# Optimization experiments

Measured on AMD Instinct MI355X. Metric: run time of the kernel, lower is better.

Reference implementation:

```python
import jax, jax.numpy as jnp
import numpy as np

VTHR = 1.0


def setup_inputs() -> dict:
    key = jax.random.key(0)
    k1, k2, k3 = jax.random.split(key, 3)
    B, T, IN, OUT = 256, 8, 4096, 4096
    x = jax.random.normal(k1, (B * T, IN), dtype=jnp.float32)
    weight_scaled = jax.random.normal(k2, (OUT, IN), dtype=jnp.float32) * 0.02
    bias_scaled = jax.random.normal(k3, (OUT,), dtype=jnp.float32) * 0.02
    return {"x": x, "weight_scaled": weight_scaled, "bias_scaled": bias_scaled, "timesteps": T}


def _spike_linear(x, weight_scaled, bias_scaled, timesteps):
    # F.linear: [B*T, IN] @ [OUT, IN]^T + [OUT]
    out = jnp.dot(x, weight_scaled.T) + bias_scaled  # [B*T, OUT]
    OUT = out.shape[-1]
    out_s = out.reshape(-1, timesteps, OUT)  # [B, T, OUT]
    out_t = jnp.transpose(out_s, (1, 0, 2))  # [T, B, OUT] for scan

    def step(memb, o_t):
        memb = memb + VTHR * o_t
        spike = (memb > VTHR).astype(out.dtype)
        memb = memb * (1.0 - spike)  # reset_mode == 'zero'
        return memb, spike

    memb0 = jnp.zeros(out_t.shape[1:], dtype=out.dtype)
    _, spikes = jax.lax.scan(step, memb0, out_t)  # [T, B, OUT]
    # torch.cat(spikes, 0): t-major concat -> [T*B, OUT]
    return spikes.reshape(-1, OUT)


def reference(x, weight_scaled, bias_scaled, timesteps):
    return _spike_linear(x, weight_scaled, bias_scaled, timesteps)
```

## Files before the change

### kernel.cpp

```cpp
#include <hip/hip_runtime.h>


typedef float v2f __attribute__((ext_vector_type(2)));

#define PK_LO(a, x, wv)                                                       \
    asm("v_pk_fma_f32 %0, %1, %2, %0 op_sel:[0,0,0] op_sel_hi:[0,1,1]"        \
        : "+v"(a) : "v"(x), "v"(wv))
#define PK_HI(a, x, wv)                                                       \
    asm("v_pk_fma_f32 %0, %1, %2, %0 op_sel:[1,0,0] op_sel_hi:[1,1,1]"        \
        : "+v"(a) : "v"(x), "v"(wv))

constexpr int TSTEPS = 8;
constexpr int BK     = 16;
constexpr int TILE_M = 64;
constexpr int TILE_NP= 256;
constexpr int TILE_N = 128;
constexpr int KC     = 384;
constexpr int WS_PAD = 4;

__global__ __launch_bounds__(256, 2)
void spike_panel_gemm(const float* __restrict__ x,
                      const float* __restrict__ w,
                      float* __restrict__ panels,
                      float* __restrict__ out,
                      int slice0, int NW,
                      int B, int IN, int OUT, int npanels)
{
    __shared__ float xs[BK][TILE_M + 4];
    __shared__ float wsh[BK][TILE_NP + WS_PAD];

    const int tid  = threadIdx.x;
    const int lane = tid & 63;
    const int wv   = tid >> 6;
    const int rg   = lane >> 3;
    const int cg   = lane & 7;
    const int clo  = wv * 64 + cg * 4;

    const int m0 = blockIdx.y * TILE_M;
    const int n0 = slice0 + blockIdx.x * TILE_NP;
    const int p  = blockIdx.z;
    const int ks = p * KC;
    const int ke = (ks + KC < IN) ? (ks + KC) : IN;

    v2f acc[TSTEPS][4];
    #pragma unroll
    for (int t = 0; t < TSTEPS; ++t)
        #pragma unroll
        for (int q = 0; q < 4; ++q) acc[t][q] = (v2f){0.f, 0.f};

    const int sr = tid >> 2;
    const int sk = (tid & 3) * 4;

    const float* xrow  = x + (size_t)(m0 + sr) * IN + sk;
    const float* wrow0 = w + (size_t)(n0 +       sr) * IN + sk;
    const float* wrow1 = w + (size_t)(n0 +  64 + sr) * IN + sk;
    const float* wrow2 = w + (size_t)(n0 + 128 + sr) * IN + sk;
    const float* wrow3 = w + (size_t)(n0 + 192 + sr) * IN + sk;

    const int nsteps = (ke - ks) / BK;

    float4 xv  = *(const float4*)(xrow  + ks);
    float4 wv0 = *(const float4*)(wrow0 + ks);
    float4 wv1 = *(const float4*)(wrow1 + ks);
    float4 wv2 = *(const float4*)(wrow2 + ks);
    float4 wv3 = *(const float4*)(wrow3 + ks);

    for (int s = 0; s < nsteps; ++s) {
        __syncthreads();
        xs[sk+0][sr] = xv.x;  xs[sk+1][sr] = xv.y;
        xs[sk+2][sr] = xv.z;  xs[sk+3][sr] = xv.w;
        wsh[sk+0][sr]     = wv0.x; wsh[sk+1][sr]     = wv0.y;
        wsh[sk+2][sr]     = wv0.z; wsh[sk+3][sr]     = wv0.w;
        wsh[sk+0][sr+64]  = wv1.x; wsh[sk+1][sr+64]  = wv1.y;
        wsh[sk+2][sr+64]  = wv1.z; wsh[sk+3][sr+64]  = wv1.w;
        wsh[sk+0][sr+128] = wv2.x; wsh[sk+1][sr+128] = wv2.y;
        wsh[sk+2][sr+128] = wv2.z; wsh[sk+3][sr+128] = wv2.w;
        wsh[sk+0][sr+192] = wv3.x; wsh[sk+1][sr+192] = wv3.y;
        wsh[sk+2][sr+192] = wv3.z; wsh[sk+3][sr+192] = wv3.w;
        __syncthreads();

        if (s + 1 < nsteps) {
            const int ko = ks + (s + 1) * BK;
            xv  = *(const float4*)(xrow  + ko);
            wv0 = *(const float4*)(wrow0 + ko);
            wv1 = *(const float4*)(wrow1 + ko);
            wv2 = *(const float4*)(wrow2 + ko);
            wv3 = *(const float4*)(wrow3 + ko);
        }

        #pragma unroll
        for (int k = 0; k < BK; ++k) {
            v2f xp[4], wva[4];
            *(float4*)&xp[0]  = *(const float4*)&xs[k][rg*8];
            *(float4*)&xp[2]  = *(const float4*)&xs[k][rg*8 + 4];
            *(float4*)&wva[0] = *(const float4*)&wsh[k][clo];
            *(float4*)&wva[2] = *(const float4*)&wsh[k][clo + 32];
            #pragma unroll
            for (int tp = 0; tp < 4; ++tp) {
                #pragma unroll
                for (int q = 0; q < 4; ++q) {
                    PK_LO(acc[2*tp  ][q], xp[tp], wva[q]);
                    PK_HI(acc[2*tp+1][q], xp[tp], wva[q]);
                }
            }
        }
    }

    const int bg = blockIdx.y * 8 + rg;
    const int cs = blockIdx.x * TILE_NP + clo;
    if (p < npanels - 1) {
        float* pb = panels + ((size_t)p * B * TSTEPS) * NW;
        #pragma unroll
        for (int t = 0; t < TSTEPS; ++t) {
            const int m = bg * TSTEPS + t;
            float4 lo, hi;
            *(v2f*)&lo.x = acc[t][0]; *(v2f*)&lo.z = acc[t][1];
            *(v2f*)&hi.x = acc[t][2]; *(v2f*)&hi.z = acc[t][3];
            *(float4*)(pb + (size_t)m * NW + cs)      = lo;
            *(float4*)(pb + (size_t)m * NW + cs + 32) = hi;
        }
    } else {
        const int o0 = n0 + clo;
        #pragma unroll
        for (int t = 0; t < TSTEPS; ++t) {
            float4 lo, hi;
            *(v2f*)&lo.x = acc[t][0]; *(v2f*)&lo.z = acc[t][1];
            *(v2f*)&hi.x = acc[t][2]; *(v2f*)&hi.z = acc[t][3];
            float* op = out + ((size_t)t * B + bg) * OUT + o0;
            *(float4*)op        = lo;
            *(float4*)(op + 32) = hi;
        }
    }
}

__global__ __launch_bounds__(256)
void spike_fold_scan(const float* __restrict__ panels,
                     const float* __restrict__ bias,
                     float* __restrict__ out,
                     int slice0, int NW,
                     int B, int OUT, int npanels)
{
    const int b = blockIdx.y;
    const size_t psz = (size_t)B * TSTEPS * NW;
    const int nc4 = NW / 4;

    for (int c4 = blockIdx.x * 256 + threadIdx.x; c4 < nc4;
         c4 += gridDim.x * 256) {
        const int cs   = c4 * 4;
        const int gcol = slice0 + cs;

        float4 v[TSTEPS];
        #pragma unroll
        for (int t = 0; t < TSTEPS; ++t)
            v[t] = *(const float4*)(panels + (size_t)(b*TSTEPS + t) * NW + cs);
        for (int p = 1; p < npanels - 1; ++p) {
            const float* pb = panels + (size_t)p * psz;
            #pragma unroll
            for (int t = 0; t < TSTEPS; ++t) {
                const float4 u = *(const float4*)(pb + (size_t)(b*TSTEPS + t) * NW + cs);
                v[t].x += u.x; v[t].y += u.y; v[t].z += u.z; v[t].w += u.w;
            }
        }
        #pragma unroll
        for (int t = 0; t < TSTEPS; ++t) {
            const float4 u = *(const float4*)(out + ((size_t)t * B + b) * OUT + gcol);
            v[t].x += u.x; v[t].y += u.y; v[t].z += u.z; v[t].w += u.w;
        }

        const float4 bb = *(const float4*)(bias + gcol);
        float memb[4] = {0.f, 0.f, 0.f, 0.f};
        #pragma unroll
        for (int t = 0; t < TSTEPS; ++t) {
            float pre[4] = {v[t].x + bb.x, v[t].y + bb.y,
                            v[t].z + bb.z, v[t].w + bb.w};
            float4 sp;
            float* spp = (float*)&sp;
            #pragma unroll
            for (int c = 0; c < 4; ++c) {
                memb[c] += pre[c];
                float s = (memb[c] > 1.0f) ? 1.0f : 0.0f;
                memb[c] *= (1.0f - s);
                spp[c] = s;
            }
            *(float4*)(out + ((size_t)t * B + b) * OUT + gcol) = sp;
        }
    }
}

__global__ __launch_bounds__(256, 4)
void spike_linear_f32seq(const float* __restrict__ x,
                         const float* __restrict__ w,
                         const float* __restrict__ bias,
                         float* __restrict__ out,
                         int B, int IN, int OUT)
{
    __shared__ float xs[BK][TILE_M + 4];
    __shared__ float ws[BK][TILE_N + 4];

    const int tid = threadIdx.x;
    const int tx  = tid & 31;
    const int ty  = tid >> 5;

    const int m0 = blockIdx.y * TILE_M;
    const int n0 = blockIdx.x * TILE_N;

    float acc_tot[TSTEPS][4];
    float acc_blk[TSTEPS][4];
    #pragma unroll
    for (int t = 0; t < TSTEPS; ++t)
        #pragma unroll
        for (int c = 0; c < 4; ++c) { acc_tot[t][c] = 0.f; acc_blk[t][c] = 0.f; }

    const int sr = tid >> 2;
    const int sk = (tid & 3) * 4;

    const float* xrow  = x + (size_t)(m0 + sr) * IN + sk;
    const float* wrow0 = w + (size_t)(n0 + sr) * IN + sk;
    const float* wrow1 = w + (size_t)(n0 + 64 + sr) * IN + sk;

    for (int kk = 0; kk < IN; kk += BK) {
        if (kk > 0 && (kk % KC) == 0) {
            #pragma unroll
            for (int t = 0; t < TSTEPS; ++t)
                #pragma unroll
                for (int c = 0; c < 4; ++c) {
                    acc_tot[t][c] += acc_blk[t][c];
                    acc_blk[t][c] = 0.f;
                }
        }
        const float4 xv  = *(const float4*)(xrow  + kk);
        const float4 wv0 = *(const float4*)(wrow0 + kk);
        const float4 wv1 = *(const float4*)(wrow1 + kk);
        __syncthreads();
        xs[sk+0][sr] = xv.x;  xs[sk+1][sr] = xv.y;
        xs[sk+2][sr] = xv.z;  xs[sk+3][sr] = xv.w;
        ws[sk+0][sr]    = wv0.x; ws[sk+1][sr]    = wv0.y;
        ws[sk+2][sr]    = wv0.z; ws[sk+3][sr]    = wv0.w;
        ws[sk+0][sr+64] = wv1.x; ws[sk+1][sr+64] = wv1.y;
        ws[sk+2][sr+64] = wv1.z; ws[sk+3][sr+64] = wv1.w;
        __syncthreads();

        #pragma unroll
        for (int k = 0; k < BK; ++k) {
            float xr[TSTEPS];
            *(float4*)&xr[0] = *(const float4*)&xs[k][ty*8];
            *(float4*)&xr[4] = *(const float4*)&xs[k][ty*8 + 4];
            float wr[4];
            *(float4*)&wr[0] = *(const float4*)&ws[k][tx*4];
            #pragma unroll
            for (int t = 0; t < TSTEPS; ++t)
                #pragma unroll
                for (int c = 0; c < 4; ++c)
                    acc_blk[t][c] = fmaf(xr[t], wr[c], acc_blk[t][c]);
        }
    }
    #pragma unroll
    for (int t = 0; t < TSTEPS; ++t)
        #pragma unroll
        for (int c = 0; c < 4; ++c)
            acc_tot[t][c] += acc_blk[t][c];

    const int bg = blockIdx.y * 8 + ty;
    const int o0 = n0 + tx * 4;
    const float4 bv = *(const float4*)(bias + o0);
    const float bb[4] = {bv.x, bv.y, bv.z, bv.w};
    float memb[4] = {0.f, 0.f, 0.f, 0.f};
    #pragma unroll
    for (int t = 0; t < TSTEPS; ++t) {
        float4 sp;
        float* spp = (float*)&sp;
        #pragma unroll
        for (int c = 0; c < 4; ++c) {
            float pre = acc_tot[t][c] + bb[c];
            memb[c] += pre;
            float s = (memb[c] > 1.0f) ? 1.0f : 0.0f;
            memb[c] *= (1.0f - s);
            spp[c] = s;
        }
        *(float4*)(out + ((size_t)t * B + bg) * OUT + o0) = sp;
    }
}

extern "C" void kernel_launch(void* const* d_in, const int* in_sizes, int n_in,
                              void* d_out, int out_size, void* d_ws, size_t ws_size,
                              hipStream_t stream)
{
    const float* x    = (const float*)d_in[0];
    const float* w    = (const float*)d_in[1];
    const float* bias = (const float*)d_in[2];
    float* out = (float*)d_out;

    const int OUT = in_sizes[2];
    const int IN  = in_sizes[1] / OUT;
    const int BT  = in_sizes[0] / IN;
    const int B   = BT / TSTEPS;

    const int npanels = (IN + KC - 1) / KC;

    int NW = 0;
    for (int cand = 4096; cand >= 256; cand >>= 1) {
        if ((OUT % cand) == 0 &&
            (size_t)(npanels - 1) * BT * cand * sizeof(float) <= ws_size) {
            NW = cand;
            break;
        }
    }

    if (NW >= 256 && npanels >= 2) {
        float* panels = (float*)d_ws;
        const int nslices = OUT / NW;
        for (int s = 0; s < nslices; ++s) {
            const int slice0 = s * NW;
            dim3 g1(NW / TILE_NP, BT / TILE_M, npanels);
            spike_panel_gemm<<<g1, 256, 0, stream>>>(x, w, panels, out,
                                                     slice0, NW, B, IN, OUT,
                                                     npanels);
            int gx = NW / 1024; if (gx < 1) gx = 1;
            dim3 g2(gx, B);
            spike_fold_scan<<<g2, 256, 0, stream>>>(panels, bias, out,
                                                    slice0, NW, B, OUT,
                                                    npanels);
        }
    } else {
        dim3 grid(OUT / TILE_N, BT / TILE_M);
        spike_linear_f32seq<<<grid, 256, 0, stream>>>(x, w, bias, out, B, IN, OUT);
    }
}
```

Measured before the change: 800.7 us.

## Double-buffer GEMM tiles with direct global-to-LDS weight loads and swizzled layout

Weight tiles are now fetched straight into LDS with global_load_lds into a double buffer stored k-contiguous per output column, using an XOR swizzle to spread bank accesses. The x tile is also double-buffered, which removes one barrier per k-step and overlaps loads with compute. The packed-FMA accumulator layout is reorganized to pair over k with timestep-paired x, and the epilogue repacks lanes. This adds register pressure and more complex indexing, and depends on the async LDS load being correctly ordered by the single barrier.

```diff
diff --git a/kernel.cpp b/kernel.cpp
--- a/kernel.cpp
+++ b/kernel.cpp
@@ -3,12 +3,12 @@
 
 typedef float v2f __attribute__((ext_vector_type(2)));
 
-#define PK_LO(a, x, wv)                                                       \
+#define PK_LO(a, w2, xp)                                                      \
     asm("v_pk_fma_f32 %0, %1, %2, %0 op_sel:[0,0,0] op_sel_hi:[0,1,1]"        \
-        : "+v"(a) : "v"(x), "v"(wv))
-#define PK_HI(a, x, wv)                                                       \
+        : "+v"(a) : "v"(w2), "v"(xp))
+#define PK_HI(a, w2, xp)                                                      \
     asm("v_pk_fma_f32 %0, %1, %2, %0 op_sel:[1,0,0] op_sel_hi:[1,1,1]"        \
-        : "+v"(a) : "v"(x), "v"(wv))
+        : "+v"(a) : "v"(w2), "v"(xp))
 
 constexpr int TSTEPS = 8;
 constexpr int BK     = 16;
@@ -16,7 +16,6 @@
 constexpr int TILE_NP= 256;
 constexpr int TILE_N = 128;
 constexpr int KC     = 384;
-constexpr int WS_PAD = 4;
 
 __global__ __launch_bounds__(256, 2)
 void spike_panel_gemm(const float* __restrict__ x,
@@ -26,14 +25,15 @@
                       int slice0, int NW,
                       int B, int IN, int OUT, int npanels)
 {
-    __shared__ float xs[BK][TILE_M + 4];
-    __shared__ float wsh[BK][TILE_NP + WS_PAD];
+    __shared__ float xs[2][BK][TILE_M + 4];
+    __shared__ float wsh[2][TILE_NP * BK];
 
     const int tid  = threadIdx.x;
     const int lane = tid & 63;
     const int wv   = tid >> 6;
     const int rg   = lane >> 3;
     const int cg   = lane & 7;
+    const int cg3  = cg & 3;
     const int clo  = wv * 64 + cg * 4;
 
     const int m0 = blockIdx.y * TILE_M;
@@ -42,67 +42,99 @@
     const int ks = p * KC;
     const int ke = (ks + KC < IN) ? (ks + KC) : IN;
 
-    v2f acc[TSTEPS][4];
-    #pragma unroll
-    for (int t = 0; t < TSTEPS; ++t)
-        #pragma unroll
-        for (int q = 0; q < 4; ++q) acc[t][q] = (v2f){0.f, 0.f};
+    v2f accp[4][8];
+    #pragma unroll
+    for (int tr = 0; tr < 4; ++tr)
+        #pragma unroll
+        for (int c = 0; c < 8; ++c) accp[tr][c] = (v2f){0.f, 0.f};
 
     const int sr = tid >> 2;
     const int sk = (tid & 3) * 4;
-
-    const float* xrow  = x + (size_t)(m0 + sr) * IN + sk;
-    const float* wrow0 = w + (size_t)(n0 +       sr) * IN + sk;
-    const float* wrow1 = w + (size_t)(n0 +  64 + sr) * IN + sk;
-    const float* wrow2 = w + (size_t)(n0 + 128 + sr) * IN + sk;
-    const float* wrow3 = w + (size_t)(n0 + 192 + sr) * IN + sk;
+    const float* xrow = x + (size_t)(m0 + sr) * IN + sk;
+
+    const int kqs = ((lane & 3) ^ ((lane >> 4) & 3)) * 4;
+    const float* wdma[4];
+    #pragma unroll
+    for (int q = 0; q < 4; ++q) {
+        const int c = (wv * 4 + q) * 16 + (lane >> 2);
+        wdma[q] = w + (size_t)(n0 + c) * IN + ks + kqs;
+    }
 
     const int nsteps = (ke - ks) / BK;
 
-    float4 xv  = *(const float4*)(xrow  + ks);
-    float4 wv0 = *(const float4*)(wrow0 + ks);
-    float4 wv1 = *(const float4*)(wrow1 + ks);
-    float4 wv2 = *(const float4*)(wrow2 + ks);
-    float4 wv3 = *(const float4*)(wrow3 + ks);
+    #pragma unroll
+    for (int q = 0; q < 4; ++q) {
+        __builtin_amdgcn_global_load_lds(
+            (const __attribute__((address_space(1))) void*)wdma[q],
+            (__attribute__((address_space(3))) void*)&wsh[0][(wv*4 + q) * 256],
+            16, 0, 0);
+        wdma[q] += BK;
+    }
+    {
+        const float4 xv0 = *(const float4*)(xrow + ks);
+        xs[0][sk+0][sr] = xv0.x;  xs[0][sk+1][sr] = xv0.y;
+        xs[0][sk+2][sr] = xv0.z;  xs[0][sk+3][sr] = xv0.w;
+    }
 
     for (int s = 0; s < nsteps; ++s) {
+        const int cur = s & 1;
         __syncthreads();
-        xs[sk+0][sr] = xv.x;  xs[sk+1][sr] = xv.y;
-        xs[sk+2][sr] = xv.z;  xs[sk+3][sr] = xv.w;
-        wsh[sk+0][sr]     = wv0.x; wsh[sk+1][sr]     = wv0.y;
-        wsh[sk+2][sr]     = wv0.z; wsh[sk+3][sr]     = wv0.w;
-        wsh[sk+0][sr+64]  = wv1.x; wsh[sk+1][sr+64]  = wv1.y;
-        wsh[sk+2][sr+64]  = wv1.z; wsh[sk+3][sr+64]  = wv1.w;
-        wsh[sk+0][sr+128] = wv2.x; wsh[sk+1][sr+128] = wv2.y;
-        wsh[sk+2][sr+128] = wv2.z; wsh[sk+3][sr+128] = wv2.w;
-        wsh[sk+0][sr+192] = wv3.x; wsh[sk+1][sr+192] = wv3.y;
-        wsh[sk+2][sr+192] = wv3.z; wsh[sk+3][sr+192] = wv3.w;
-        __syncthreads();
-
-        if (s + 1 < nsteps) {
-            const int ko = ks + (s + 1) * BK;
-            xv  = *(const float4*)(xrow  + ko);
-            wv0 = *(const float4*)(wrow0 + ko);
-            wv1 = *(const float4*)(wrow1 + ko);
-            wv2 = *(const float4*)(wrow2 + ko);
-            wv3 = *(const float4*)(wrow3 + ko);
-        }
-
-        #pragma unroll
-        for (int k = 0; k < BK; ++k) {
-            v2f xp[4], wva[4];
-            *(float4*)&xp[0]  = *(const float4*)&xs[k][rg*8];
-            *(float4*)&xp[2]  = *(const float4*)&xs[k][rg*8 + 4];
-            *(float4*)&wva[0] = *(const float4*)&wsh[k][clo];
-            *(float4*)&wva[2] = *(const float4*)&wsh[k][clo + 32];
-            #pragma unroll
-            for (int tp = 0; tp < 4; ++tp) {
+
+        const bool hn = (s + 1) < nsteps;
+        float4 xv;
+        if (hn) {
+            #pragma unroll
+            for (int q = 0; q < 4; ++q) {
+                __builtin_amdgcn_global_load_lds(
+                    (const __attribute__((address_space(1))) void*)wdma[q],
+                    (__attribute__((address_space(3))) void*)
+                        &wsh[cur ^ 1][(wv*4 + q) * 256],
+                    16, 0, 0);
+                wdma[q] += BK;
+            }
+            xv = *(const float4*)(xrow + ks + (s + 1) * BK);
+        }
+
+        #pragma unroll
+        for (int kq = 0; kq < 4; ++kq) {
+            const int woff = ((kq ^ cg3) << 2);
+            float4 wq0[4], wq1[4];
+            #pragma unroll
+            for (int j = 0; j < 4; ++j) {
+                wq0[j] = *(const float4*)&wsh[cur][(clo + j) * 16 + woff];
+                wq1[j] = *(const float4*)&wsh[cur][(clo + 32 + j) * 16 + woff];
+            }
+            #pragma unroll
+            for (int k2 = 0; k2 < 4; ++k2) {
+                const int k = kq * 4 + k2;
+                const float4 xa = *(const float4*)&xs[cur][k][rg * 8];
+                const float4 xb = *(const float4*)&xs[cur][k][rg * 8 + 4];
+                v2f xp[4];
+                xp[0] = (v2f){xa.x, xa.y}; xp[1] = (v2f){xa.z, xa.w};
+                xp[2] = (v2f){xb.x, xb.y}; xp[3] = (v2f){xb.z, xb.w};
                 #pragma unroll
-                for (int q = 0; q < 4; ++q) {
-                    PK_LO(acc[2*tp  ][q], xp[tp], wva[q]);
-                    PK_HI(acc[2*tp+1][q], xp[tp], wva[q]);
+                for (int j = 0; j < 4; ++j) {
+                    const v2f* w0 = (const v2f*)&wq0[j];
+                    const v2f* w1 = (const v2f*)&wq1[j];
+                    #pragma unroll
+                    for (int tr = 0; tr < 4; ++tr) {
+                        if (k2 == 0) { PK_LO(accp[tr][j],     w0[0], xp[tr]);
+                                       PK_LO(accp[tr][4 + j], w1[0], xp[tr]); }
+                        if (k2 == 1) { PK_HI(accp[tr][j],     w0[0], xp[tr]);
+                                       PK_HI(accp[tr][4 + j], w1[0], xp[tr]); }
+                        if (k2 == 2) { PK_LO(accp[tr][j],     w0[1], xp[tr]);
+                                       PK_LO(accp[tr][4 + j], w1[1], xp[tr]); }
+                        if (k2 == 3) { PK_HI(accp[tr][j],     w0[1], xp[tr]);
+                                       PK_HI(accp[tr][4 + j], w1[1], xp[tr]); }
+                    }
                 }
             }
+        }
+
+        if (hn) {
+            const int nb = cur ^ 1;
+            xs[nb][sk+0][sr] = xv.x;  xs[nb][sk+1][sr] = xv.y;
+            xs[nb][sk+2][sr] = xv.z;  xs[nb][sk+3][sr] = xv.w;
         }
     }
 
@@ -112,10 +144,20 @@
         float* pb = panels + ((size_t)p * B * TSTEPS) * NW;
         #pragma unroll
         for (int t = 0; t < TSTEPS; ++t) {
+            const int tr = t >> 1;
+            float4 lo, hi;
+            if (t & 1) {
+                lo = (float4){accp[tr][0].y, accp[tr][1].y,
+                              accp[tr][2].y, accp[tr][3].y};
+                hi = (float4){accp[tr][4].y, accp[tr][5].y,
+                              accp[tr][6].y, accp[tr][7].y};
+            } else {
+                lo = (float4){accp[tr][0].x, accp[tr][1].x,
+                              accp[tr][2].x, accp[tr][3].x};
+                hi = (float4){accp[tr][4].x, accp[tr][5].x,
+                              accp[tr][6].x, accp[tr][7].x};
+            }
             const int m = bg * TSTEPS + t;
-            float4 lo, hi;
-            *(v2f*)&lo.x = acc[t][0]; *(v2f*)&lo.z = acc[t][1];
-            *(v2f*)&hi.x = acc[t][2]; *(v2f*)&hi.z = acc[t][3];
             *(float4*)(pb + (size_t)m * NW + cs)      = lo;
             *(float4*)(pb + (size_t)m * NW + cs + 32) = hi;
         }
@@ -123,9 +165,19 @@
         const int o0 = n0 + clo;
         #pragma unroll
         for (int t = 0; t < TSTEPS; ++t) {
+            const int tr = t >> 1;
             float4 lo, hi;
-            *(v2f*)&lo.x = acc[t][0]; *(v2f*)&lo.z = acc[t][1];
-            *(v2f*)&hi.x = acc[t][2]; *(v2f*)&hi.z = acc[t][3];
+            if (t & 1) {
+                lo = (float4){accp[tr][0].y, accp[tr][1].y,
+                              accp[tr][2].y, accp[tr][3].y};
+                hi = (float4){accp[tr][4].y, accp[tr][5].y,
+                              accp[tr][6].y, accp[tr][7].y};
+            } else {
+                lo = (float4){accp[tr][0].x, accp[tr][1].x,
+                              accp[tr][2].x, accp[tr][3].x};
+                hi = (float4){accp[tr][4].x, accp[tr][5].x,
+                              accp[tr][6].x, accp[tr][7].x};
+            }
             float* op = out + ((size_t)t * B + bg) * OUT + o0;
             *(float4*)op        = lo;
             *(float4*)(op + 32) = hi;
```

New measurement: 809.3 us. About the same (+1.1%).
